# Kernel tuning notes

Measured on AMD Instinct MI355X. Metric: run time of the kernel, lower is better.

The kernel has to match this reference:

```python
import jax, jax.numpy as jnp
import numpy as np
from jax import lax

# ---- model dims ----
NTOKEN = 60697
D_MODEL = 512
NLAYERS = 4
D_STATE = 16
D_CONV = 4
EXPAND = 2
D_INNER = EXPAND * D_MODEL      # 1024
DT_RANK = (D_MODEL + 15) // 16  # 32 (ceil(d_model/16), mamba default)
B_SZ = 4
SEQ = 2048
EPS = 1e-5


def setup_inputs() -> dict:
    key = jax.random.key(0)
    ks = jax.random.split(key, 16)
    s = 0.02
    src = jax.random.randint(ks[0], (B_SZ, SEQ), 0, NTOKEN)
    src_key_padding_mask = jnp.ones((B_SZ, SEQ), dtype=bool)
    emb_w = jax.random.normal(ks[1], (NTOKEN, D_MODEL), jnp.float32) * s
    enc_ln_w = jnp.ones((D_MODEL,), jnp.float32)
    enc_ln_b = jnp.zeros((D_MODEL,), jnp.float32)
    ln_w = jnp.ones((NLAYERS, D_MODEL), jnp.float32)
    ln_b = jnp.zeros((NLAYERS, D_MODEL), jnp.float32)
    in_proj_w = jax.random.normal(ks[2], (NLAYERS, 2 * D_INNER, D_MODEL), jnp.float32) * s
    conv_w = jax.random.normal(ks[3], (NLAYERS, D_INNER, D_CONV), jnp.float32) * 0.1
    conv_b = jnp.zeros((NLAYERS, D_INNER), jnp.float32)
    x_proj_w = jax.random.normal(ks[4], (NLAYERS, DT_RANK + 2 * D_STATE, D_INNER), jnp.float32) * s
    dt_proj_w = jax.random.normal(ks[5], (NLAYERS, D_INNER, DT_RANK), jnp.float32) * (DT_RANK ** -0.5)
    dt_proj_b = jax.random.uniform(ks[6], (NLAYERS, D_INNER), jnp.float32, -4.0, -2.0)
    # S4D real init: A = -[1..d_state], stored as log
    A_log = jnp.log(jnp.broadcast_to(jnp.arange(1, D_STATE + 1, dtype=jnp.float32),
                                     (NLAYERS, D_INNER, D_STATE)))
    D_skip = jnp.ones((NLAYERS, D_INNER), jnp.float32)
    out_proj_w = jax.random.normal(ks[7], (NLAYERS, D_MODEL, D_INNER), jnp.float32) * s / np.sqrt(NLAYERS)
    normf_w = jnp.ones((D_MODEL,), jnp.float32)
    normf_b = jnp.zeros((D_MODEL,), jnp.float32)
    return {
        'src': src, 'src_key_padding_mask': src_key_padding_mask,
        'emb_w': emb_w, 'enc_ln_w': enc_ln_w, 'enc_ln_b': enc_ln_b,
        'ln_w': ln_w, 'ln_b': ln_b, 'in_proj_w': in_proj_w,
        'conv_w': conv_w, 'conv_b': conv_b, 'x_proj_w': x_proj_w,
        'dt_proj_w': dt_proj_w, 'dt_proj_b': dt_proj_b,
        'A_log': A_log, 'D_skip': D_skip, 'out_proj_w': out_proj_w,
        'normf_w': normf_w, 'normf_b': normf_b,
    }


def _layer_norm(x, w, b, eps=EPS):
    mu = jnp.mean(x, axis=-1, keepdims=True)
    var = jnp.mean(jnp.square(x - mu), axis=-1, keepdims=True)
    return (x - mu) * lax.rsqrt(var + eps) * w + b


def _mamba_mixer(h, in_w, cw, cb, xw, dtw, dtb, A_log, D_skip, ow):
    B, L, _ = h.shape
    xz = h @ in_w.T                                   # [B,L,2*d_inner]
    x, z = jnp.split(xz, 2, axis=-1)
    # causal depthwise conv1d, kernel D_CONV
    xt = x.swapaxes(1, 2)                             # [B,d_inner,L]
    xp = jnp.pad(xt, ((0, 0), (0, 0), (D_CONV - 1, 0)))
    conv = cb[None, :, None]
    for k in range(D_CONV):
        conv = conv + cw[:, k][None, :, None] * xp[:, :, k:k + L]
    x = jax.nn.silu(conv).swapaxes(1, 2)              # [B,L,d_inner]
    xdbl = x @ xw.T                                   # [B,L,dt_rank+2*d_state]
    dt = jax.nn.softplus(xdbl[..., :DT_RANK] @ dtw.T + dtb)      # [B,L,d_inner]
    Bm = xdbl[..., DT_RANK:DT_RANK + D_STATE]                    # [B,L,d_state]
    Cm = xdbl[..., DT_RANK + D_STATE:]                           # [B,L,d_state]
    A = -jnp.exp(A_log)                               # [d_inner,d_state]

    def step(hst, inp):
        dt_t, b_t, c_t, x_t = inp                     # [B,d_inner],[B,d_state],[B,d_state],[B,d_inner]
        dA = jnp.exp(dt_t[..., None] * A)             # [B,d_inner,d_state]
        hst = dA * hst + (dt_t * x_t)[..., None] * b_t[:, None, :]
        y_t = jnp.einsum('bds,bs->bd', hst, c_t)
        return hst, y_t

    xs = (dt.swapaxes(0, 1), Bm.swapaxes(0, 1), Cm.swapaxes(0, 1), x.swapaxes(0, 1))
    h0 = jnp.zeros((B, D_INNER, D_STATE), dtype=h.dtype)
    _, ys = lax.scan(step, h0, xs)                    # ys: [L,B,d_inner]
    y = ys.swapaxes(0, 1) + x * D_skip
    y = y * jax.nn.silu(z)
    return y @ ow.T


def reference(src, src_key_padding_mask, emb_w, enc_ln_w, enc_ln_b, ln_w, ln_b,
              in_proj_w, conv_w, conv_b, x_proj_w, dt_proj_w, dt_proj_b,
              A_log, D_skip, out_proj_w, normf_w, normf_b):
    # GeneEncoder: embedding -> LayerNorm (dropout = identity in eval)
    hidden = _layer_norm(emb_w[src], enc_ln_w, enc_ln_b)
    residual = None
    for i in range(NLAYERS):  # prenorm Mamba Blocks
        residual = hidden if residual is None else hidden + residual
        hidden = _mamba_mixer(_layer_norm(residual, ln_w[i], ln_b[i]),
                              in_proj_w[i], conv_w[i], conv_b[i], x_proj_w[i],
                              dt_proj_w[i], dt_proj_b[i], A_log[i], D_skip[i],
                              out_proj_w[i])
    residual = hidden + residual
    return _layer_norm(residual, normf_w, normf_b)
```

## Files before the change

kernel.cpp:

```cpp
#include <hip/hip_runtime.h>
#include <hip/hip_bf16.h>
#include <math.h>

#define NTOKEN 60697
#define D_MODEL 512
#define NLAYERS 4
#define D_STATE 16
#define D_CONV 4
#define D_INNER 1024
#define DT_RANK 32
#define B_SZ 4
#define SEQ 2048
#define EPS 1e-5f
#define NROWS (B_SZ * SEQ)
#define CHUNK 128
#define NCHUNK (SEQ / CHUNK)
#define LOG2E 1.44269504f

typedef __bf16 bf16_t;
typedef __attribute__((ext_vector_type(8))) __bf16 bfx8;
typedef __attribute__((ext_vector_type(4))) __bf16 bfx4;
typedef __attribute__((ext_vector_type(4))) float f32x4;


__device__ __forceinline__ float fast_sigmoid(float x) {
    return 1.0f / (1.0f + __expf(-x));
}
__device__ __forceinline__ float silu(float x) {
    return x * fast_sigmoid(x);
}
__device__ __forceinline__ float softplus_f(float x) {
    return (x > 20.0f) ? x : log1pf(__expf(x));
}
__device__ __forceinline__ float exp2_fast(float x) {
    float r;
    asm("v_exp_f32 %0, %1" : "=v"(r) : "v"(x));
    return r;
}
__device__ __forceinline__ unsigned int bf16bits(float v) {
    return (unsigned int)__builtin_bit_cast(unsigned short, (bf16_t)v);
}
__device__ __forceinline__ float lo16f(unsigned int u) {
    return __builtin_bit_cast(float, u << 16);
}
__device__ __forceinline__ float hi16f(unsigned int u) {
    return __builtin_bit_cast(float, u & 0xFFFF0000u);
}

__device__ __forceinline__ void gload_lds16(const void* g, void* l) {
    __builtin_amdgcn_global_load_lds(
        (const __attribute__((address_space(1))) unsigned int*)g,
        (__attribute__((address_space(3))) unsigned int*)l, 16, 0, 0);
}

template <int CTRL>
__device__ __forceinline__ float dpp_fetch(float x) {
    int xi = __builtin_bit_cast(int, x);
    int yi = __builtin_amdgcn_update_dpp(0, xi, CTRL, 0xF, 0xF, true);
    return __builtin_bit_cast(float, yi);
}
__device__ __forceinline__ float dpp_sum16(float p) {
    p += dpp_fetch<0xB1>(p);
    p += dpp_fetch<0x4E>(p);
    p += dpp_fetch<0x141>(p);
    p += dpp_fetch<0x140>(p);
    return p;
}

__device__ __forceinline__ float blk_reduce_sum(float x, float* sbuf) {
#pragma unroll
    for (int m = 32; m >= 1; m >>= 1) x += __shfl_xor(x, m);
    int wid = threadIdx.x >> 6;
    if ((threadIdx.x & 63) == 0) sbuf[wid] = x;
    __syncthreads();
    float t = sbuf[0] + sbuf[1] + sbuf[2] + sbuf[3];
    __syncthreads();
    return t;
}

__global__ __launch_bounds__(256) void cast_all_kernel(
    const float* __restrict__ s0, const float* __restrict__ s1,
    const float* __restrict__ s2, const float* __restrict__ s3,
    bf16_t* __restrict__ d0, bf16_t* __restrict__ d1,
    bf16_t* __restrict__ d2, bf16_t* __restrict__ d3,
    size_t n0, size_t n1, size_t n2, size_t n3)
{
    size_t ntot = n0 + n1 + n2 + n3;
    size_t stride = (size_t)gridDim.x * 256 * 4;
    for (size_t i = ((size_t)blockIdx.x * 256 + threadIdx.x) * 4; i < ntot; i += stride) {
        const float* s; bf16_t* dst; size_t off = i;
        if (off < n0) { s = s0; dst = d0; }
        else if ((off -= n0) < n1) { s = s1; dst = d1; }
        else if ((off -= n1) < n2) { s = s2; dst = d2; }
        else { off -= n2; s = s3; dst = d3; }
        float4 v = *reinterpret_cast<const float4*>(s + off);
        bfx4 o;
        o[0] = (bf16_t)v.x; o[1] = (bf16_t)v.y;
        o[2] = (bf16_t)v.z; o[3] = (bf16_t)v.w;
        *reinterpret_cast<bfx4*>(dst + off) = o;
    }
}


__global__ __launch_bounds__(256) void embed_ln_kernel(
    const int* __restrict__ src, const float* __restrict__ emb,
    const float* __restrict__ w, const float* __restrict__ b,
    float* __restrict__ R)
{
    __shared__ float sbuf[4];
    int row = blockIdx.x;
    int tok = src[row];
    const float* e = emb + (size_t)tok * D_MODEL;
    int c0 = threadIdx.x, c1 = threadIdx.x + 256;
    float v0 = e[c0], v1 = e[c1];
    float mu = blk_reduce_sum(v0 + v1, sbuf) * (1.0f / D_MODEL);
    float d0 = v0 - mu, d1 = v1 - mu;
    float var = blk_reduce_sum(d0 * d0 + d1 * d1, sbuf) * (1.0f / D_MODEL);
    float rs = rsqrtf(var + EPS);
    size_t base = (size_t)row * D_MODEL;
    R[base + c0] = d0 * rs * w[c0] + b[c0];
    R[base + c1] = d1 * rs * w[c1] + b[c1];
}

__global__ __launch_bounds__(256) void add_ln_kernel(
    float* __restrict__ R, const float* __restrict__ Hadd,
    const float* __restrict__ w, const float* __restrict__ b,
    float* __restrict__ out, bf16_t* __restrict__ outb)
{
    __shared__ float sbuf[4];
    size_t base = (size_t)blockIdx.x * D_MODEL;
    int c0 = threadIdx.x, c1 = c0 + 256;
    float v0 = R[base + c0], v1 = R[base + c1];
    if (Hadd) {
        v0 += Hadd[base + c0];
        v1 += Hadd[base + c1];
        R[base + c0] = v0;
        R[base + c1] = v1;
    }
    float mu = blk_reduce_sum(v0 + v1, sbuf) * (1.0f / D_MODEL);
    float d0 = v0 - mu, d1 = v1 - mu;
    float var = blk_reduce_sum(d0 * d0 + d1 * d1, sbuf) * (1.0f / D_MODEL);
    float rs = rsqrtf(var + EPS);
    float o0 = d0 * rs * w[c0] + b[c0];
    float o1 = d1 * rs * w[c1] + b[c1];
    if (out) {
        out[base + c0] = o0;
        out[base + c1] = o1;
    }
    if (outb) {
        outb[base + c0] = (bf16_t)o0;
        outb[base + c1] = (bf16_t)o1;
    }
}

template <int EPI>
__global__ __launch_bounds__(256) void gemm_bf16_nt(
    const bf16_t* __restrict__ A, const bf16_t* __restrict__ B,
    float* __restrict__ C, int ldc, int K, const float* __restrict__ bias,
    const unsigned short* __restrict__ xcb_u16,
    unsigned int* __restrict__ dtx_u32,
    bf16_t* __restrict__ Cxb, bf16_t* __restrict__ Czb)
{
    __shared__ bf16_t As[128 * 32];
    __shared__ bf16_t Bs[128 * 32];
    int tid = threadIdx.x;
    int lane = tid & 63, wid = tid >> 6;
    int m0 = blockIdx.y * 128, n0 = blockIdx.x * 128;
    int wm = (wid >> 1) * 64, wn = (wid & 1) * 64;
    int c_lo = lane & 15;
    int khalf = lane >> 4;

    f32x4 acc[4][4];
#pragma unroll
    for (int i = 0; i < 4; i++)
#pragma unroll
        for (int j = 0; j < 4; j++)
            acc[i][j] = (f32x4){0.f, 0.f, 0.f, 0.f};

    for (int k0 = 0; k0 < K; k0 += 32) {
#pragma unroll
        for (int i = 0; i < 2; i++) {
            int c = i * 256 + tid;
            int row = c >> 2;
            int cb = (c & 3) * 16;
            int ldsoff = (i * 256 + wid * 64) * 16;
            gload_lds16((const char*)A + ((size_t)(m0 + row) * K + k0) * 2 + cb,
                        (char*)As + ldsoff);
            gload_lds16((const char*)B + ((size_t)(n0 + row) * K + k0) * 2 + cb,
                        (char*)Bs + ldsoff);
        }
        __syncthreads();

        bfx8 af[4], bfr[4];
#pragma unroll
        for (int i = 0; i < 4; i++) {
            af[i]  = *reinterpret_cast<const bfx8*>(As + (wm + i * 16 + c_lo) * 32 + khalf * 8);
            bfr[i] = *reinterpret_cast<const bfx8*>(Bs + (wn + i * 16 + c_lo) * 32 + khalf * 8);
        }
#pragma unroll
        for (int i = 0; i < 4; i++)
#pragma unroll
            for (int j = 0; j < 4; j++)
                acc[i][j] = __builtin_amdgcn_mfma_f32_16x16x32_bf16(af[i], bfr[j], acc[i][j], 0, 0, 0);
        __syncthreads();
    }

#pragma unroll
    for (int i = 0; i < 4; i++) {
#pragma unroll
        for (int j = 0; j < 4; j++) {
            int row0 = m0 + wm + i * 16 + khalf * 4;
            int col = n0 + wn + j * 16 + c_lo;
#pragma unroll
            for (int r = 0; r < 4; r++) {
                int row = row0 + r;
                float v = acc[i][j][r];
                if (EPI == 0) {
                    C[(size_t)row * ldc + col] = v;
                } else if (EPI == 2) {
                    v = softplus_f(v + bias[col]);
                    float xf = lo16f((unsigned int)xcb_u16[(size_t)row * D_INNER + col]);
                    unsigned int u = bf16bits(v) | (bf16bits(v * xf) << 16);
                    dtx_u32[(size_t)(row >> 1) * 2048 + col * 2 + (row & 1)] = u;
                } else if (EPI == 3) {
                    if (col < D_INNER) Cxb[(size_t)row * D_INNER + col] = (bf16_t)v;
                    else               Czb[(size_t)row * D_INNER + col - D_INNER] = (bf16_t)v;
                }
            }
        }
    }
}

__global__ __launch_bounds__(128) void gemm_xp_bf16(
    const bf16_t* __restrict__ A, const bf16_t* __restrict__ Bmat,
    bf16_t* __restrict__ XDlow, unsigned int* __restrict__ BCb, int K)
{
    __shared__ bf16_t As[64 * 32];
    __shared__ bf16_t Bs[64 * 32];
    int tid = threadIdx.x;
    int lane = tid & 63, w = tid >> 6;
    int m0 = blockIdx.x * 64;
    int wr0 = w * 32;
    int c_lo = lane & 15;
    int khalf = lane >> 4;

    f32x4 acc[2][4];
#pragma unroll
    for (int i = 0; i < 2; i++)
#pragma unroll
        for (int j = 0; j < 4; j++)
            acc[i][j] = (f32x4){0.f, 0.f, 0.f, 0.f};

    for (int k0 = 0; k0 < K; k0 += 32) {
#pragma unroll
        for (int call = 0; call < 2; call++) {
            int c = call * 128 + tid;
            int base = (call * 128 + w * 64) * 16;
            gload_lds16((const char*)A + ((size_t)(m0 + (c >> 2)) * K + k0) * 2 + (c & 3) * 16,
                        (char*)As + base);
            gload_lds16((const char*)Bmat + ((size_t)(c >> 2) * K + k0) * 2 + (c & 3) * 16,
                        (char*)Bs + base);
        }
        __syncthreads();

        bfx8 af[2], bfr[4];
#pragma unroll
        for (int i = 0; i < 2; i++)
            af[i] = *reinterpret_cast<const bfx8*>(As + (wr0 + i * 16 + c_lo) * 32 + khalf * 8);
#pragma unroll
        for (int j = 0; j < 4; j++)
            bfr[j] = *reinterpret_cast<const bfx8*>(Bs + (j * 16 + c_lo) * 32 + khalf * 8);
#pragma unroll
        for (int i = 0; i < 2; i++)
#pragma unroll
            for (int j = 0; j < 4; j++)
                acc[i][j] = __builtin_amdgcn_mfma_f32_16x16x32_bf16(af[i], bfr[j], acc[i][j], 0, 0, 0);
        __syncthreads();
    }

#pragma unroll
    for (int i = 0; i < 2; i++) {
        int row0 = m0 + wr0 + i * 16 + khalf * 4;
#pragma unroll
        for (int r = 0; r < 4; r++) {
            int row = row0 + r;
            XDlow[(size_t)row * DT_RANK + c_lo]      = (bf16_t)acc[i][0][r];
            XDlow[(size_t)row * DT_RANK + 16 + c_lo] = (bf16_t)acc[i][1][r];
            unsigned int u = bf16bits(acc[i][2][r]) | (bf16bits(acc[i][3][r]) << 16);
            BCb[(size_t)(row >> 1) * 32 + c_lo * 2 + (row & 1)] = u;
        }
    }
}

__global__ __launch_bounds__(256) void conv_silu_kernel(
    const bf16_t* __restrict__ Xrawb, const float* __restrict__ cw,
    const float* __restrict__ cb, bf16_t* __restrict__ XCb)
{
    size_t gid = (size_t)blockIdx.x * 256 + threadIdx.x;
    int dp = (int)(gid & 511);
    size_t bt = gid >> 9;
    int t = (int)(bt & (SEQ - 1));
    const unsigned int* Xu = (const unsigned int*)Xrawb;
    int d0 = 2 * dp;
    float a0 = cb[d0], a1 = cb[d0 + 1];
#pragma unroll
    for (int k = 0; k < D_CONV; k++) {
        int tt = t + k - (D_CONV - 1);
        if (tt >= 0) {
            unsigned int u = Xu[(bt + (size_t)(k - (D_CONV - 1))) * 512 + dp];
            a0 += cw[d0 * D_CONV + k] * lo16f(u);
            a1 += cw[(d0 + 1) * D_CONV + k] * hi16f(u);
        }
    }
    unsigned int o = bf16bits(silu(a0)) | (bf16bits(silu(a1)) << 16);
    ((unsigned int*)XCb)[gid] = o;
}

__device__ __forceinline__ void scan_stage64(
    char* base, const unsigned int* __restrict__ DTXp,
    const unsigned int* __restrict__ BCp, size_t rowpair0, int d0, int tid)
{
    gload_lds16(DTXp + (rowpair0 + (size_t)(tid >> 3)) * 2048 + d0 * 2 + (tid & 7) * 4,
                base + tid * 16);
    gload_lds16(BCp + rowpair0 * 32 + tid * 4, base + 4096 + tid * 16);
}

__global__ __launch_bounds__(256) void scan_pA_kernel(
    const unsigned int* __restrict__ DTXb, const unsigned int* __restrict__ BCb,
    const float* __restrict__ A_log,
    float* __restrict__ DcB, float* __restrict__ UcB)
{
    __shared__ __align__(16) char lds[2][8192];
    const int tid = threadIdx.x;
    const int s = tid & 15, dl = tid >> 4;
    const int b = blockIdx.x >> 6;
    const int d0 = (blockIdx.x & 63) * 16;
    const int c = blockIdx.y;
    const int d = d0 + dl;
    const float Av2 = -__expf(A_log[d * D_STATE + s]) * LOG2E;
    const size_t bbase = (size_t)b * SEQ;
    const int tstart = c * CHUNK;

    float h = 0.f, cum = 0.f;
    scan_stage64(lds[0], DTXb, BCb, (bbase + tstart) >> 1, d0, tid);
    __syncthreads();
    int cur = 0;
    for (int t0 = 0; t0 < CHUNK; t0 += 64) {
        if (t0 + 64 < CHUNK)
            scan_stage64(lds[cur ^ 1], DTXb, BCb, (bbase + tstart + t0 + 64) >> 1, d0, tid);
        const char* L = lds[cur];
#pragma unroll
        for (int kk2 = 0; kk2 < 32; kk2++) {
            uint2 dp = *(const uint2*)(L + kk2 * 128 + dl * 8);
            uint2 bp = *(const uint2*)(L + 4096 + kk2 * 128 + s * 8);
#pragma unroll
            for (int j = 0; j < 2; j++) {
                unsigned int pk = j ? dp.y : dp.x;
                unsigned int bk = j ? bp.y : bp.x;
                float dtv = lo16f(pk);
                float ux  = hi16f(pk);
                float bv  = lo16f(bk);
                float e = exp2_fast(dtv * Av2);
                h = fmaf(e, h, ux * bv);
                cum += dtv;
            }
        }
        __syncthreads();
        cur ^= 1;
    }
    size_t cb64 = ((size_t)c * B_SZ + b) * D_INNER + d;
    UcB[cb64 * 16 + s] = h;
    if (s == 0) DcB[cb64] = cum;
}

__global__ __launch_bounds__(256) void scan_p2_kernel(
    const float* __restrict__ A_log, const float* __restrict__ DcB,
    const float* __restrict__ UcB, float* __restrict__ HcB)
{
    int tid = threadIdx.x;
    int s = tid & 15, dl = tid >> 4;
    int chain = blockIdx.x * 16 + dl;
    int b = chain >> 10, d = chain & 1023;
    float Av = -__expf(A_log[d * D_STATE + s]);
    float Hv = 0.f;
    for (int c = 0; c < NCHUNK; c++) {
        size_t base = ((size_t)c * B_SZ + b) * D_INNER + d;
        HcB[base * 16 + s] = Hv;
        Hv = __expf(Av * DcB[base]) * Hv + UcB[base * 16 + s];
    }
}

__global__ __launch_bounds__(256) void scan_pB_kernel(
    const unsigned int* __restrict__ DTXb, const unsigned int* __restrict__ BCb,
    const float* __restrict__ HcB, const float* __restrict__ A_log,
    const bf16_t* __restrict__ Zbufb, const float* __restrict__ Dskip,
    bf16_t* __restrict__ XCb)
{
    __shared__ __align__(16) char lds[2][8192];
    __shared__ float ytile[32][17];
    const int tid = threadIdx.x;
    const int s = tid & 15, dl = tid >> 4;
    const int b = blockIdx.x >> 6;
    const int d0 = (blockIdx.x & 63) * 16;
    const int c = blockIdx.y;
    const int d = d0 + dl;
    const float Av2 = -__expf(A_log[d * D_STATE + s]) * LOG2E;
    const size_t bbase = (size_t)b * SEQ;
    const int tstart = c * CHUNK;

    float h = HcB[(((size_t)c * B_SZ + b) * D_INNER + d) * 16 + s];

    const int tl  = tid >> 3;
    const int dlo = (tid * 2) & 15;
    const float dsk0 = Dskip[d0 + dlo];
    const float dsk1 = Dskip[d0 + dlo + 1];

    scan_stage64(lds[0], DTXb, BCb, (bbase + tstart) >> 1, d0, tid);
    __syncthreads();
    int cur = 0;
    for (int t0 = 0; t0 < CHUNK; t0 += 64) {
        if (t0 + 64 < CHUNK)
            scan_stage64(lds[cur ^ 1], DTXb, BCb, (bbase + tstart + t0 + 64) >> 1, d0, tid);
        const char* L = lds[cur];
#pragma unroll
        for (int g = 0; g < 2; g++) {
#pragma unroll
            for (int half = 0; half < 2; half++) {
                float yhold = 0.f;
#pragma unroll
                for (int k8 = 0; k8 < 8; k8++) {
                    int kk2 = g * 16 + half * 8 + k8;
                    uint2 dp = *(const uint2*)(L + kk2 * 128 + dl * 8);
                    uint2 bp = *(const uint2*)(L + 4096 + kk2 * 128 + s * 8);
#pragma unroll
                    for (int j = 0; j < 2; j++) {
                        unsigned int pk = j ? dp.y : dp.x;
                        unsigned int bk = j ? bp.y : bp.x;
                        float dtv = lo16f(pk);
                        float ux  = hi16f(pk);
                        float bv  = lo16f(bk);
                        float cv  = hi16f(bk);
                        float e = exp2_fast(dtv * Av2);
                        h = fmaf(e, h, ux * bv);
                        float p = dpp_sum16(h * cv);
                        int k16 = k8 * 2 + j;
                        if (s == k16) yhold = p;
                    }
                }
                ytile[half * 16 + s][dl] = yhold;
            }
            __syncthreads();
            {
                int t = tstart + t0 + g * 32 + tl;
                size_t row = (bbase + t) * (size_t)D_INNER + d0 + dlo;
                float y0 = ytile[tl][dlo];
                float y1 = ytile[tl][dlo + 1];
                unsigned int xw = *(const unsigned int*)(XCb + row);
                unsigned int zw = *(const unsigned int*)(Zbufb + row);
                float g0 = (y0 + lo16f(xw) * dsk0) * silu(lo16f(zw));
                float g1 = (y1 + hi16f(xw) * dsk1) * silu(hi16f(zw));
                unsigned int o = bf16bits(g0) | (bf16bits(g1) << 16);
                *(unsigned int*)(XCb + row) = o;
            }
            __syncthreads();
        }
        cur ^= 1;
    }
}


extern "C" void kernel_launch(void* const* d_in, const int* in_sizes, int n_in,
                              void* d_out, int out_size, void* d_ws, size_t ws_size,
                              hipStream_t stream) {
    const int*   src       = (const int*)d_in[0];
    const float* emb_w     = (const float*)d_in[2];
    const float* enc_ln_w  = (const float*)d_in[3];
    const float* enc_ln_b  = (const float*)d_in[4];
    const float* ln_w      = (const float*)d_in[5];
    const float* ln_b      = (const float*)d_in[6];
    const float* in_proj_w = (const float*)d_in[7];
    const float* conv_w    = (const float*)d_in[8];
    const float* conv_b    = (const float*)d_in[9];
    const float* x_proj_w  = (const float*)d_in[10];
    const float* dt_proj_w = (const float*)d_in[11];
    const float* dt_proj_b = (const float*)d_in[12];
    const float* A_log     = (const float*)d_in[13];
    const float* D_skip    = (const float*)d_in[14];
    const float* out_proj_w= (const float*)d_in[15];
    const float* normf_w   = (const float*)d_in[16];
    const float* normf_b   = (const float*)d_in[17];
    float* out = (float*)d_out;

    float* R    = (float*)d_ws;
    float* H    = R    + (size_t)NROWS * D_MODEL;
    float* DcB  = H    + (size_t)NROWS * D_MODEL;
    float* UcB  = DcB  + (size_t)NCHUNK * B_SZ * D_INNER;
    float* HcB  = UcB  + (size_t)NCHUNK * B_SZ * D_INNER * D_STATE;
    unsigned int* BCb = (unsigned int*)(HcB + (size_t)NCHUNK * B_SZ * D_INNER * D_STATE);
    unsigned int* DTXb = BCb + (size_t)(NROWS / 2) * 32;
    bf16_t* Hb    = (bf16_t*)(DTXb + (size_t)(NROWS / 2) * 2048);
    bf16_t* Xrawb = Hb    + (size_t)NROWS * D_MODEL;
    bf16_t* Zbufb = Xrawb + (size_t)NROWS * D_INNER;
    bf16_t* XCb   = Zbufb + (size_t)NROWS * D_INNER;
    bf16_t* XDlow = XCb   + (size_t)NROWS * D_INNER;
    bf16_t* Wib   = XDlow + (size_t)NROWS * DT_RANK;
    bf16_t* Wob   = Wib   + (size_t)NLAYERS * 2 * D_INNER * D_MODEL;
    bf16_t* xpb   = Wob   + (size_t)NLAYERS * D_MODEL * D_INNER;
    bf16_t* dtwb  = xpb   + (size_t)NLAYERS * 64 * D_INNER;

    cast_all_kernel<<<2048, 256, 0, stream>>>(
        in_proj_w, out_proj_w, x_proj_w, dt_proj_w,
        Wib, Wob, xpb, dtwb,
        (size_t)NLAYERS * 2 * D_INNER * D_MODEL,
        (size_t)NLAYERS * D_MODEL * D_INNER,
        (size_t)NLAYERS * 64 * D_INNER,
        (size_t)NLAYERS * D_INNER * DT_RANK);

    embed_ln_kernel<<<NROWS, 256, 0, stream>>>(src, emb_w, enc_ln_w, enc_ln_b, R);

    for (int L = 0; L < NLAYERS; L++) {
        const float* AlogL = A_log + (size_t)L * D_INNER * D_STATE;

        add_ln_kernel<<<NROWS, 256, 0, stream>>>(
            R, (L == 0) ? nullptr : H, ln_w + L * D_MODEL, ln_b + L * D_MODEL,
            nullptr, Hb);

        gemm_bf16_nt<3><<<dim3(16, 64), 256, 0, stream>>>(
            Hb, Wib + (size_t)L * 2 * D_INNER * D_MODEL, nullptr, 0, D_MODEL,
            nullptr, nullptr, nullptr, Xrawb, Zbufb);

        conv_silu_kernel<<<(NROWS * D_INNER / 2) / 256, 256, 0, stream>>>(
            Xrawb, conv_w + (size_t)L * D_INNER * D_CONV, conv_b + (size_t)L * D_INNER, XCb);

        gemm_xp_bf16<<<NROWS / 64, 128, 0, stream>>>(
            XCb, xpb + (size_t)L * 64 * D_INNER, XDlow, BCb, D_INNER);

        gemm_bf16_nt<2><<<dim3(8, 64), 256, 0, stream>>>(
            XDlow, dtwb + (size_t)L * D_INNER * DT_RANK, nullptr, 0, DT_RANK,
            dt_proj_b + (size_t)L * D_INNER, (const unsigned short*)XCb, DTXb,
            nullptr, nullptr);

        scan_pA_kernel<<<dim3(B_SZ * 64, NCHUNK), 256, 0, stream>>>(
            DTXb, BCb, AlogL, DcB, UcB);
        scan_p2_kernel<<<256, 256, 0, stream>>>(AlogL, DcB, UcB, HcB);
        scan_pB_kernel<<<dim3(B_SZ * 64, NCHUNK), 256, 0, stream>>>(
            DTXb, BCb, HcB, AlogL, Zbufb, D_skip + (size_t)L * D_INNER, XCb);

        gemm_bf16_nt<0><<<dim3(4, 64), 256, 0, stream>>>(
            XCb, Wob + (size_t)L * D_MODEL * D_INNER, H, D_MODEL, D_INNER,
            nullptr, nullptr, nullptr, nullptr, nullptr);
    }

    add_ln_kernel<<<NROWS, 256, 0, stream>>>(R, H, normf_w, normf_b, out, nullptr);
}
```

Before: 1.169 ms.

## Fuse residual add into out-proj GEMM and fold chunk-prefix scan into pB

The out-projection GEMM now accumulates directly into the residual buffer, so the per-layer LayerNorm no longer reads a separate H buffer or writes R back, and the H buffer is dropped. The sequential inter-chunk scan kernel is removed. Each scan_pB block instead recomputes its own initial state by looping over all preceding chunk summaries, issued after the LDS staging load so the two can overlap. This saves one launch and the HcB round trip per layer, at the cost of redundant O(NCHUNK) prefix work in later chunks and read-modify-write traffic in the GEMM epilogue.

Result: no change. 1.185 ms (+1.4%).

```diff
diff --git a/kernel.cpp b/kernel.cpp
--- a/kernel.cpp
+++ b/kernel.cpp
@@ -122,8 +122,8 @@
     R[base + c1] = d1 * rs * w[c1] + b[c1];
 }
 
-__global__ __launch_bounds__(256) void add_ln_kernel(
-    float* __restrict__ R, const float* __restrict__ Hadd,
+__global__ __launch_bounds__(256) void ln_kernel(
+    const float* __restrict__ R,
     const float* __restrict__ w, const float* __restrict__ b,
     float* __restrict__ out, bf16_t* __restrict__ outb)
 {
@@ -131,12 +131,6 @@
     size_t base = (size_t)blockIdx.x * D_MODEL;
     int c0 = threadIdx.x, c1 = c0 + 256;
     float v0 = R[base + c0], v1 = R[base + c1];
-    if (Hadd) {
-        v0 += Hadd[base + c0];
-        v1 += Hadd[base + c1];
-        R[base + c0] = v0;
-        R[base + c1] = v1;
-    }
     float mu = blk_reduce_sum(v0 + v1, sbuf) * (1.0f / D_MODEL);
     float d0 = v0 - mu, d1 = v1 - mu;
     float var = blk_reduce_sum(d0 * d0 + d1 * d1, sbuf) * (1.0f / D_MODEL);
@@ -215,8 +209,9 @@
             for (int r = 0; r < 4; r++) {
                 int row = row0 + r;
                 float v = acc[i][j][r];
-                if (EPI == 0) {
-                    C[(size_t)row * ldc + col] = v;
+                if (EPI == 4) {
+                    size_t idx = (size_t)row * ldc + col;
+                    C[idx] += v;
                 } else if (EPI == 2) {
                     v = softplus_f(v + bias[col]);
                     float xf = lo16f((unsigned int)xcb_u16[(size_t)row * D_INNER + col]);
@@ -373,26 +368,10 @@
     if (s == 0) DcB[cb64] = cum;
 }
 
-__global__ __launch_bounds__(256) void scan_p2_kernel(
-    const float* __restrict__ A_log, const float* __restrict__ DcB,
-    const float* __restrict__ UcB, float* __restrict__ HcB)
-{
-    int tid = threadIdx.x;
-    int s = tid & 15, dl = tid >> 4;
-    int chain = blockIdx.x * 16 + dl;
-    int b = chain >> 10, d = chain & 1023;
-    float Av = -__expf(A_log[d * D_STATE + s]);
-    float Hv = 0.f;
-    for (int c = 0; c < NCHUNK; c++) {
-        size_t base = ((size_t)c * B_SZ + b) * D_INNER + d;
-        HcB[base * 16 + s] = Hv;
-        Hv = __expf(Av * DcB[base]) * Hv + UcB[base * 16 + s];
-    }
-}
-
 __global__ __launch_bounds__(256) void scan_pB_kernel(
     const unsigned int* __restrict__ DTXb, const unsigned int* __restrict__ BCb,
-    const float* __restrict__ HcB, const float* __restrict__ A_log,
+    const float* __restrict__ DcB, const float* __restrict__ UcB,
+    const float* __restrict__ A_log,
     const bf16_t* __restrict__ Zbufb, const float* __restrict__ Dskip,
     bf16_t* __restrict__ XCb)
 {
@@ -408,14 +387,19 @@
     const size_t bbase = (size_t)b * SEQ;
     const int tstart = c * CHUNK;
 
-    float h = HcB[(((size_t)c * B_SZ + b) * D_INNER + d) * 16 + s];
+    scan_stage64(lds[0], DTXb, BCb, (bbase + tstart) >> 1, d0, tid);
+
+    float h = 0.f;
+    for (int j = 0; j < c; j++) {
+        size_t base = ((size_t)j * B_SZ + b) * D_INNER + d;
+        h = exp2_fast(Av2 * DcB[base]) * h + UcB[base * 16 + s];
+    }
 
     const int tl  = tid >> 3;
     const int dlo = (tid * 2) & 15;
     const float dsk0 = Dskip[d0 + dlo];
     const float dsk1 = Dskip[d0 + dlo + 1];
 
-    scan_stage64(lds[0], DTXb, BCb, (bbase + tstart) >> 1, d0, tid);
     __syncthreads();
     int cur = 0;
     for (int t0 = 0; t0 < CHUNK; t0 += 64) {
@@ -492,11 +476,9 @@
     float* out = (float*)d_out;
 
     float* R    = (float*)d_ws;
-    float* H    = R    + (size_t)NROWS * D_MODEL;
-    float* DcB  = H    + (size_t)NROWS * D_MODEL;
+    float* DcB  = R    + (size_t)NROWS * D_MODEL;
     float* UcB  = DcB  + (size_t)NCHUNK * B_SZ * D_INNER;
-    float* HcB  = UcB  + (size_t)NCHUNK * B_SZ * D_INNER * D_STATE;
-    unsigned int* BCb = (unsigned int*)(HcB + (size_t)NCHUNK * B_SZ * D_INNER * D_STATE);
+    unsigned int* BCb = (unsigned int*)(UcB + (size_t)NCHUNK * B_SZ * D_INNER * D_STATE);
     unsigned int* DTXb = BCb + (size_t)(NROWS / 2) * 32;
     bf16_t* Hb    = (bf16_t*)(DTXb + (size_t)(NROWS / 2) * 2048);
     bf16_t* Xrawb = Hb    + (size_t)NROWS * D_MODEL;
@@ -521,9 +503,8 @@
     for (int L = 0; L < NLAYERS; L++) {
         const float* AlogL = A_log + (size_t)L * D_INNER * D_STATE;
 
-        add_ln_kernel<<<NROWS, 256, 0, stream>>>(
-            R, (L == 0) ? nullptr : H, ln_w + L * D_MODEL, ln_b + L * D_MODEL,
-            nullptr, Hb);
+        ln_kernel<<<NROWS, 256, 0, stream>>>(
+            R, ln_w + L * D_MODEL, ln_b + L * D_MODEL, nullptr, Hb);
 
         gemm_bf16_nt<3><<<dim3(16, 64), 256, 0, stream>>>(
             Hb, Wib + (size_t)L * 2 * D_INNER * D_MODEL, nullptr, 0, D_MODEL,
@@ -542,14 +523,13 @@
 
         scan_pA_kernel<<<dim3(B_SZ * 64, NCHUNK), 256, 0, stream>>>(
             DTXb, BCb, AlogL, DcB, UcB);
-        scan_p2_kernel<<<256, 256, 0, stream>>>(AlogL, DcB, UcB, HcB);
         scan_pB_kernel<<<dim3(B_SZ * 64, NCHUNK), 256, 0, stream>>>(
-            DTXb, BCb, HcB, AlogL, Zbufb, D_skip + (size_t)L * D_INNER, XCb);
-
-        gemm_bf16_nt<0><<<dim3(4, 64), 256, 0, stream>>>(
-            XCb, Wob + (size_t)L * D_MODEL * D_INNER, H, D_MODEL, D_INNER,
+            DTXb, BCb, DcB, UcB, AlogL, Zbufb, D_skip + (size_t)L * D_INNER, XCb);
+
+        gemm_bf16_nt<4><<<dim3(4, 64), 256, 0, stream>>>(
+            XCb, Wob + (size_t)L * D_MODEL * D_INNER, R, D_MODEL, D_INNER,
             nullptr, nullptr, nullptr, nullptr, nullptr);
     }
 
-    add_ln_kernel<<<NROWS, 256, 0, stream>>>(R, H, normf_w, normf_b, out, nullptr);
-}
+    ln_kernel<<<NROWS, 256, 0, stream>>>(R, normf_w, normf_b, out, nullptr);
+}
```
